# Kernel tuning notes

Hardware: AMD Instinct MI355X
Metric: run time of the kernel (lower is better)

Reference implementation:

```python
import jax, jax.numpy as jnp
import numpy as np

B, OBJ, INP, HID = 8, 128, 64, 256
D = 3 * INP  # concatenated per-object feature dim


def setup_inputs() -> dict:
    key = jax.random.key(0)
    ks = jax.random.split(key, 12)
    s = 0.02
    return {
        "x0": jax.random.normal(ks[0], (B, OBJ, INP), jnp.float32),
        "x1": jax.random.normal(ks[1], (B, OBJ, INP), jnp.float32),
        "x2": jax.random.normal(ks[2], (B, OBJ, INP), jnp.float32),
        # weights stored [in, out] so forward is x @ w + b
        "w_enc": jax.random.normal(ks[3], (2 * D, HID), jnp.float32) * s,
        "b_enc": jnp.zeros((HID,), jnp.float32),
        "w1": jax.random.normal(ks[4], (HID, HID), jnp.float32) * s,
        "b1": jnp.zeros((HID,), jnp.float32),
        "w2": jax.random.normal(ks[5], (HID, HID), jnp.float32) * s,
        "b2": jnp.zeros((HID,), jnp.float32),
        "w3": jax.random.normal(ks[6], (HID, HID), jnp.float32) * s,
        "b3": jnp.zeros((HID,), jnp.float32),
        "wd1": jax.random.normal(ks[7], (HID, HID), jnp.float32) * s,
        "bd1": jnp.zeros((HID,), jnp.float32),
        "wd2": jax.random.normal(ks[8], (HID, INP), jnp.float32) * s,
        "bd2": jnp.zeros((INP,), jnp.float32),
    }


def reference(x0, x1, x2, w_enc, b_enc, w1, b1, w2, b2, w3, b3, wd1, bd1, wd2, bd2):
    x = jnp.concatenate([x0, x1, x2], axis=-1)  # [B, N, D]
    # Fused equivalent of Linear(cat(e1, e2)): split w_enc rows into the part
    # acting on the first-object features and the second-object features, then
    # broadcast-add instead of materializing the [B,N,N,2D] concat tensor.
    ea = jnp.einsum("bnd,dh->bnh", x, w_enc[:D])   # acts on data_e1
    eb = jnp.einsum("bnd,dh->bnh", x, w_enc[D:])   # acts on data_e2
    h = jax.nn.relu(ea[:, :, None, :] + eb[:, None, :, :] + b_enc)  # [B,N,N,H]
    h = jax.nn.relu(h @ w1 + b1)
    h = jax.nn.relu(h @ w2 + b2)
    h = h @ w3 + b3              # fc3 has no activation before the mean
    pooled = h.mean(axis=2)      # [B, N, H]
    out = jax.nn.relu(pooled @ wd1 + bd1) @ wd2 + bd2  # [B, N, INP]
    return out
```

## Files before the change

kernel.cpp:

```cpp
#include <hip/hip_runtime.h>
#include <stdint.h>


#define HID 256
#define NOBJ 128
#define NROW 1024

typedef __attribute__((ext_vector_type(8))) short short8;
typedef __attribute__((ext_vector_type(4))) float float4v;
typedef __attribute__((ext_vector_type(16))) float float16v;
typedef __attribute__((ext_vector_type(2))) unsigned int uint2v;

__device__ __forceinline__ unsigned int f2bf_u(float f) {
    unsigned int u = __builtin_bit_cast(unsigned int, f);
    u += 0x7fffu + ((u >> 16) & 1u);
    return u >> 16;
}
__device__ __forceinline__ unsigned int pack2(float a, float b) {
    return f2bf_u(a) | (f2bf_u(b) << 16);
}
__device__ __forceinline__ float relu(float v) { return v > 0.f ? v : 0.f; }

__device__ __forceinline__ void lds_barrier() {
    asm volatile("s_waitcnt lgkmcnt(0)\n\ts_barrier" ::: "memory");
}

__global__ void setup_kernel(const float* __restrict__ x0, const float* __restrict__ x1,
                             const float* __restrict__ x2, const float* __restrict__ w_enc,
                             const float* __restrict__ b_enc,
                             const float* __restrict__ w1, const float* __restrict__ w2,
                             const float* __restrict__ w3,
                             unsigned short* __restrict__ wt,
                             float* __restrict__ ea, float* __restrict__ eb) {
    const int bx = blockIdx.x, t = threadIdx.x;
    __shared__ float lw[256][33];
    __shared__ float xs[2][192];
    if (bx < 24) {
        const int m = bx >> 3, tau = bx & 7;
        const float* w = (m == 0) ? w1 : (m == 1) ? w2 : w3;
        const int n = t & 31, kk = t >> 5;
#pragma unroll
        for (int rep = 0; rep < 32; ++rep) {
            int k = rep * 8 + kk;
            lw[k][n] = w[k * 256 + tau * 32 + n];
        }
        __syncthreads();
        unsigned short* outp = wt + (m * 8 + tau) * 8192;
        const int lane = t & 63, wq = t >> 6;
        const int h5 = lane >> 5, l31n = lane & 31;
#pragma unroll
        for (int rep = 0; rep < 4; ++rep) {
            const int kb = wq * 4 + rep;
            short8 v;
#pragma unroll
            for (int e = 0; e < 8; ++e)
                v[e] = (short)f2bf_u(lw[kb * 16 + h5 * 8 + e][l31n]);
            *(short8*)(outp + kb * 512 + lane * 8) = v;
        }
        return;
    }
    const int e = bx - 24;
    for (int idx = t; idx < 384; idx += 256) {
        int r = idx / 192, d = idx % 192;
        int row = e * 2 + r;
        float v = (d < 64) ? x0[row * 64 + d]
                : (d < 128) ? x1[row * 64 + d - 64]
                : x2[row * 64 + d - 128];
        xs[r][d] = v;
    }
    __syncthreads();
    float aA[2] = {0.f, 0.f}, aB[2] = {0.f, 0.f};
#pragma unroll 16
    for (int d = 0; d < 192; ++d) {
        float wa = w_enc[d * 256 + t];
        float wb = w_enc[(192 + d) * 256 + t];
#pragma unroll
        for (int r = 0; r < 2; ++r) { aA[r] += xs[r][d] * wa; aB[r] += xs[r][d] * wb; }
    }
    float be = b_enc[t];
#pragma unroll
    for (int r = 0; r < 2; ++r) {
        ea[(e * 2 + r) * 256 + t] = aA[r] + be;
        eb[(e * 2 + r) * 256 + t] = aB[r];
    }
}

__global__ __launch_bounds__(256, 2) void pair_kernel(
        const float* __restrict__ ea, const float* __restrict__ eb,
        const unsigned short* __restrict__ wt,
        const float* __restrict__ b1, const float* __restrict__ b2,
        const float* __restrict__ b3,
        const float* __restrict__ wd1, const float* __restrict__ bd1,
        const float* __restrict__ wd2, const float* __restrict__ bd2,
        float* __restrict__ out) {
    __shared__ __align__(16) unsigned short hbuf[128 * 256];

    const int w = blockIdx.x, b = w >> 7;
    const int t = threadIdx.x, wv = t >> 6, lane = t & 63;
    const int l31 = lane & 31, h5 = lane >> 5;
    const int n0 = wv * 64;

    const unsigned short* aptr = wt + lane * 8;

    short8 af[2][2], bfr[2][4];
    af[0][0] = *(const short8*)(aptr + ((wv * 2 + 0) * 16) * 512);
    af[0][1] = *(const short8*)(aptr + ((wv * 2 + 1) * 16) * 512);

    {
        const float4v va = *(const float4v*)(ea + w * 256 + lane * 4);
        const float* ebbase = eb + (b * NOBJ) * 256;
        const int c = lane >> 1, sub = (lane & 1) * 4;
#pragma unroll 4
        for (int jj = 0; jj < 32; ++jj) {
            const int j = wv * 32 + jj;
            float4v vb = *(const float4v*)(ebbase + j * 256 + lane * 4);
            int addr = j * 256 + ((c ^ (j & 31)) << 3) + sub;
            *(uint2v*)(hbuf + addr) = (uint2v){
                pack2(relu(va[0] + vb[0]), relu(va[1] + vb[1])),
                pack2(relu(va[2] + vb[2]), relu(va[3] + vb[3]))};
        }
    }
    lds_barrier();

    int jb[4];
#pragma unroll
    for (int tj = 0; tj < 4; ++tj) jb[tj] = (tj * 32 + l31) * 256;
#pragma unroll
    for (int tj = 0; tj < 4; ++tj)
        bfr[0][tj] = *(const short8*)(hbuf + jb[tj] + ((h5 ^ l31) << 3));

    float16v acc[2][4];

#pragma unroll
    for (int l = 0; l < 3; ++l) {
        const float* bias = (l == 0) ? b1 : (l == 1) ? b2 : b3;
#pragma unroll
        for (int tn = 0; tn < 2; ++tn)
#pragma unroll
            for (int q = 0; q < 4; ++q) {
                float4v bv = *(const float4v*)(bias + n0 + tn * 32 + q * 8 + h5 * 4);
#pragma unroll
                for (int i = 0; i < 4; ++i)
#pragma unroll
                    for (int tj = 0; tj < 4; ++tj)
                        acc[tn][tj][q * 4 + i] = bv[i];
            }
#pragma unroll
        for (int kb = 0; kb < 16; ++kb) {
            const int g = l * 16 + kb, gp = g + 1;
            if (gp < 48) {
                const int lp = gp >> 4, kp = gp & 15;
                af[gp & 1][0] = *(const short8*)(aptr + ((lp * 8 + wv * 2 + 0) * 16 + kp) * 512);
                af[gp & 1][1] = *(const short8*)(aptr + ((lp * 8 + wv * 2 + 1) * 16 + kp) * 512);
            }
            if (kb < 15) {
                const int off = ((((kb + 1) * 2 + h5) ^ l31) << 3);
#pragma unroll
                for (int tj = 0; tj < 4; ++tj)
                    bfr[(kb + 1) & 1][tj] = *(const short8*)(hbuf + jb[tj] + off);
            }
#pragma unroll
            for (int tn = 0; tn < 2; ++tn)
#pragma unroll
                for (int tj = 0; tj < 4; ++tj)
                    acc[tn][tj] = __builtin_amdgcn_mfma_f32_32x32x16_bf16(
                        af[g & 1][tn], bfr[kb & 1][tj], acc[tn][tj], 0, 0, 0);
        }
        lds_barrier();

        if (l < 2) {
#pragma unroll
            for (int tn = 0; tn < 2; ++tn)
#pragma unroll
                for (int q = 0; q < 4; ++q) {
                    const int nb_ = n0 + tn * 32 + 8 * q + 4 * h5;
                    const int cn = nb_ >> 3, sub = nb_ & 7;
#pragma unroll
                    for (int tj = 0; tj < 4; ++tj) {
                        const int j = tj * 32 + l31;
                        int addr = j * 256 + ((cn ^ l31) << 3) + sub;
                        *(uint2v*)(hbuf + addr) = (uint2v){
                            pack2(relu(acc[tn][tj][q * 4]), relu(acc[tn][tj][q * 4 + 1])),
                            pack2(relu(acc[tn][tj][q * 4 + 2]), relu(acc[tn][tj][q * 4 + 3]))};
                    }
                }
            lds_barrier();
#pragma unroll
            for (int tj = 0; tj < 4; ++tj)
                bfr[0][tj] = *(const short8*)(hbuf + jb[tj] + ((h5 ^ l31) << 3));
        }
    }

    float* fs = (float*)hbuf;
    {
#pragma unroll
        for (int tn = 0; tn < 2; ++tn)
#pragma unroll
            for (int r = 0; r < 16; ++r) {
                float s = acc[tn][0][r] + acc[tn][1][r] + acc[tn][2][r] + acc[tn][3][r];
                s += __shfl_xor(s, 1);
                s += __shfl_xor(s, 2);
                s += __shfl_xor(s, 4);
                s += __shfl_xor(s, 8);
                s += __shfl_xor(s, 16);
                if (l31 == 0) {
                    const int n = n0 + tn * 32 + (r & 3) + 8 * (r >> 2) + 4 * h5;
                    fs[n] = s * 0.0078125f;
                }
            }
    }
    __syncthreads();
    {
        float a1 = bd1[t];
#pragma unroll 16
        for (int k = 0; k < 256; ++k) a1 += fs[k] * wd1[k * 256 + t];
        __syncthreads();
        fs[256 + t] = relu(a1);
    }
    __syncthreads();
    {
        const int o = lane;
        float p = 0.f;
        const float* w2p = wd2 + (wv * 64) * 64 + o;
#pragma unroll 16
        for (int kk = 0; kk < 64; ++kk) p += fs[256 + wv * 64 + kk] * w2p[kk * 64];
        fs[512 + wv * 64 + o] = p;
    }
    __syncthreads();
    if (t < 64)
        out[w * 64 + t] = fs[512 + t] + fs[576 + t] + fs[640 + t] + fs[704 + t] + bd2[t];
}

extern "C" void kernel_launch(void* const* d_in, const int* in_sizes, int n_in,
                              void* d_out, int out_size, void* d_ws, size_t ws_size,
                              hipStream_t stream) {
    const float* x0    = (const float*)d_in[0];
    const float* x1    = (const float*)d_in[1];
    const float* x2    = (const float*)d_in[2];
    const float* w_enc = (const float*)d_in[3];
    const float* b_enc = (const float*)d_in[4];
    const float* w1    = (const float*)d_in[5];
    const float* b1    = (const float*)d_in[6];
    const float* w2    = (const float*)d_in[7];
    const float* b2    = (const float*)d_in[8];
    const float* w3    = (const float*)d_in[9];
    const float* b3    = (const float*)d_in[10];
    const float* wd1   = (const float*)d_in[11];
    const float* bd1   = (const float*)d_in[12];
    const float* wd2   = (const float*)d_in[13];
    const float* bd2   = (const float*)d_in[14];
    float* out = (float*)d_out;

    unsigned short* wt = (unsigned short*)d_ws;
    float* ea = (float*)((char*)d_ws + 3 * 65536 * sizeof(unsigned short));
    float* eb = ea + NROW * HID;

    setup_kernel<<<536, 256, 0, stream>>>(x0, x1, x2, w_enc, b_enc, w1, w2, w3, wt, ea, eb);
    pair_kernel<<<NROW, 256, 0, stream>>>(ea, eb, wt, b1, b2, b3,
                                          wd1, bd1, wd2, bd2, out);
}
```

Measured before the change: 167.6 us.

## Fold fc3 past the mean pool and premultiply w3 with wd1

Because fc3 has no activation before the mean, the mean over partner objects is taken over the relu'd layer-2 output. The result is multiplied by a precomputed W34 = w3 @ wd1 with bias b34 = b3 @ wd1 + bd1. This removes the third per-pair 256x256 MFMA layer and its LDS write-back from the pair kernel, leaving two layers. The setup kernel gains 257 extra blocks to compute W34 and b34 in fp32. Numerics change slightly because the fc3 contribution is no longer bf16-rounded per pair.

```diff
diff --git a/kernel.cpp b/kernel.cpp
--- a/kernel.cpp
+++ b/kernel.cpp
@@ -29,15 +29,17 @@
                              const float* __restrict__ x2, const float* __restrict__ w_enc,
                              const float* __restrict__ b_enc,
                              const float* __restrict__ w1, const float* __restrict__ w2,
-                             const float* __restrict__ w3,
+                             const float* __restrict__ w3, const float* __restrict__ b3,
+                             const float* __restrict__ wd1, const float* __restrict__ bd1,
                              unsigned short* __restrict__ wt,
-                             float* __restrict__ ea, float* __restrict__ eb) {
+                             float* __restrict__ ea, float* __restrict__ eb,
+                             float* __restrict__ W34, float* __restrict__ b34) {
     const int bx = blockIdx.x, t = threadIdx.x;
     __shared__ float lw[256][33];
     __shared__ float xs[2][192];
-    if (bx < 24) {
+    if (bx < 16) {
         const int m = bx >> 3, tau = bx & 7;
-        const float* w = (m == 0) ? w1 : (m == 1) ? w2 : w3;
+        const float* w = (m == 0) ? w1 : w2;
         const int n = t & 31, kk = t >> 5;
 #pragma unroll
         for (int rep = 0; rep < 32; ++rep) {
@@ -59,29 +61,46 @@
         }
         return;
     }
-    const int e = bx - 24;
-    for (int idx = t; idx < 384; idx += 256) {
-        int r = idx / 192, d = idx % 192;
-        int row = e * 2 + r;
-        float v = (d < 64) ? x0[row * 64 + d]
-                : (d < 128) ? x1[row * 64 + d - 64]
-                : x2[row * 64 + d - 128];
-        xs[r][d] = v;
-    }
-    __syncthreads();
-    float aA[2] = {0.f, 0.f}, aB[2] = {0.f, 0.f};
+    if (bx < 528) {
+        const int e = bx - 16;
+        for (int idx = t; idx < 384; idx += 256) {
+            int r = idx / 192, d = idx % 192;
+            int row = e * 2 + r;
+            float v = (d < 64) ? x0[row * 64 + d]
+                    : (d < 128) ? x1[row * 64 + d - 64]
+                    : x2[row * 64 + d - 128];
+            xs[r][d] = v;
+        }
+        __syncthreads();
+        float aA[2] = {0.f, 0.f}, aB[2] = {0.f, 0.f};
 #pragma unroll 16
-    for (int d = 0; d < 192; ++d) {
-        float wa = w_enc[d * 256 + t];
-        float wb = w_enc[(192 + d) * 256 + t];
-#pragma unroll
-        for (int r = 0; r < 2; ++r) { aA[r] += xs[r][d] * wa; aB[r] += xs[r][d] * wb; }
-    }
-    float be = b_enc[t];
-#pragma unroll
-    for (int r = 0; r < 2; ++r) {
-        ea[(e * 2 + r) * 256 + t] = aA[r] + be;
-        eb[(e * 2 + r) * 256 + t] = aB[r];
+        for (int d = 0; d < 192; ++d) {
+            float wa = w_enc[d * 256 + t];
+            float wb = w_enc[(192 + d) * 256 + t];
+#pragma unroll
+            for (int r = 0; r < 2; ++r) { aA[r] += xs[r][d] * wa; aB[r] += xs[r][d] * wb; }
+        }
+        float be = b_enc[t];
+#pragma unroll
+        for (int r = 0; r < 2; ++r) {
+            ea[(e * 2 + r) * 256 + t] = aA[r] + be;
+            eb[(e * 2 + r) * 256 + t] = aB[r];
+        }
+        return;
+    }
+    if (bx < 784) {
+        const int m = bx - 528;
+        float a = 0.f;
+#pragma unroll 8
+        for (int k = 0; k < 256; ++k) a += w3[m * 256 + k] * wd1[k * 256 + t];
+        W34[m * 256 + t] = a;
+        return;
+    }
+    {
+        float a = bd1[t];
+#pragma unroll 8
+        for (int k = 0; k < 256; ++k) a += b3[k] * wd1[k * 256 + t];
+        b34[t] = a;
     }
 }
 
@@ -89,8 +108,7 @@
         const float* __restrict__ ea, const float* __restrict__ eb,
         const unsigned short* __restrict__ wt,
         const float* __restrict__ b1, const float* __restrict__ b2,
-        const float* __restrict__ b3,
-        const float* __restrict__ wd1, const float* __restrict__ bd1,
+        const float* __restrict__ W34, const float* __restrict__ b34,
         const float* __restrict__ wd2, const float* __restrict__ bd2,
         float* __restrict__ out) {
     __shared__ __align__(16) unsigned short hbuf[128 * 256];
@@ -132,8 +150,8 @@
     float16v acc[2][4];
 
 #pragma unroll
-    for (int l = 0; l < 3; ++l) {
-        const float* bias = (l == 0) ? b1 : (l == 1) ? b2 : b3;
+    for (int l = 0; l < 2; ++l) {
+        const float* bias = (l == 0) ? b1 : b2;
 #pragma unroll
         for (int tn = 0; tn < 2; ++tn)
 #pragma unroll
@@ -148,7 +166,7 @@
 #pragma unroll
         for (int kb = 0; kb < 16; ++kb) {
             const int g = l * 16 + kb, gp = g + 1;
-            if (gp < 48) {
+            if (gp < 32) {
                 const int lp = gp >> 4, kp = gp & 15;
                 af[gp & 1][0] = *(const short8*)(aptr + ((lp * 8 + wv * 2 + 0) * 16 + kp) * 512);
                 af[gp & 1][1] = *(const short8*)(aptr + ((lp * 8 + wv * 2 + 1) * 16 + kp) * 512);
@@ -168,7 +186,7 @@
         }
         lds_barrier();
 
-        if (l < 2) {
+        if (l == 0) {
 #pragma unroll
             for (int tn = 0; tn < 2; ++tn)
 #pragma unroll
@@ -197,7 +215,8 @@
         for (int tn = 0; tn < 2; ++tn)
 #pragma unroll
             for (int r = 0; r < 16; ++r) {
-                float s = acc[tn][0][r] + acc[tn][1][r] + acc[tn][2][r] + acc[tn][3][r];
+                float s = relu(acc[tn][0][r]) + relu(acc[tn][1][r])
+                        + relu(acc[tn][2][r]) + relu(acc[tn][3][r]);
                 s += __shfl_xor(s, 1);
                 s += __shfl_xor(s, 2);
                 s += __shfl_xor(s, 4);
@@ -211,24 +230,34 @@
     }
     __syncthreads();
     {
-        float a1 = bd1[t];
-#pragma unroll 16
-        for (int k = 0; k < 256; ++k) a1 += fs[k] * wd1[k * 256 + t];
-        __syncthreads();
-        fs[256 + t] = relu(a1);
-    }
-    __syncthreads();
-    {
-        const int o = lane;
+        float p0 = 0.f, p1 = 0.f, p2 = 0.f, p3 = 0.f;
+        const float* wp = W34 + (wv * 64) * 256 + lane;
+#pragma unroll 8
+        for (int kk = 0; kk < 64; ++kk) {
+            float mv = fs[wv * 64 + kk];
+            p0 += mv * wp[kk * 256];
+            p1 += mv * wp[kk * 256 + 64];
+            p2 += mv * wp[kk * 256 + 128];
+            p3 += mv * wp[kk * 256 + 192];
+        }
+        fs[256 + wv * 256 + lane]       = p0;
+        fs[256 + wv * 256 + 64 + lane]  = p1;
+        fs[256 + wv * 256 + 128 + lane] = p2;
+        fs[256 + wv * 256 + 192 + lane] = p3;
+    }
+    __syncthreads();
+    fs[1280 + t] = relu(fs[256 + t] + fs[512 + t] + fs[768 + t] + fs[1024 + t] + b34[t]);
+    __syncthreads();
+    {
         float p = 0.f;
-        const float* w2p = wd2 + (wv * 64) * 64 + o;
-#pragma unroll 16
-        for (int kk = 0; kk < 64; ++kk) p += fs[256 + wv * 64 + kk] * w2p[kk * 64];
-        fs[512 + wv * 64 + o] = p;
+        const float* w2p = wd2 + (wv * 64) * 64 + lane;
+#pragma unroll 8
+        for (int kk = 0; kk < 64; ++kk) p += fs[1280 + wv * 64 + kk] * w2p[kk * 64];
+        fs[1536 + wv * 64 + lane] = p;
     }
     __syncthreads();
     if (t < 64)
-        out[w * 64 + t] = fs[512 + t] + fs[576 + t] + fs[640 + t] + fs[704 + t] + bd2[t];
+        out[w * 64 + t] = fs[1536 + t] + fs[1600 + t] + fs[1664 + t] + fs[1728 + t] + bd2[t];
 }
 
 extern "C" void kernel_launch(void* const* d_in, const int* in_sizes, int n_in,
@@ -252,10 +281,12 @@
     float* out = (float*)d_out;
 
     unsigned short* wt = (unsigned short*)d_ws;
-    float* ea = (float*)((char*)d_ws + 3 * 65536 * sizeof(unsigned short));
-    float* eb = ea + NROW * HID;
-
-    setup_kernel<<<536, 256, 0, stream>>>(x0, x1, x2, w_enc, b_enc, w1, w2, w3, wt, ea, eb);
-    pair_kernel<<<NROW, 256, 0, stream>>>(ea, eb, wt, b1, b2, b3,
-                                          wd1, bd1, wd2, bd2, out);
-}
+    float* ea  = (float*)((char*)d_ws + 3 * 65536 * sizeof(unsigned short));
+    float* eb  = ea + NROW * HID;
+    float* W34 = eb + NROW * HID;
+    float* b34 = W34 + 256 * 256;
+
+    setup_kernel<<<785, 256, 0, stream>>>(x0, x1, x2, w_enc, b_enc, w1, w2,
+                                          w3, b3, wd1, bd1, wt, ea, eb, W34, b34);
+    pair_kernel<<<NROW, 256, 0, stream>>>(ea, eb, wt, b1, b2, W34, b34, wd2, bd2, out);
+}
```

Result: faster. 155.4 us, median of 2 (-7.3%).
